# Kernel tuning notes

Hardware: AMD Instinct MI355X
Metric: run time of the kernel (lower is better)

## Reference

```python
import jax, jax.numpy as jnp
from jax import lax
import numpy as np

B, T, C, W = 128, 64, 64, 27
H, K = 128, 3
EPS = 1e-5


def _conv1d(x, w, b):
    # x: (N, Cin, W), w: (Cout, Cin, K) -> (N, Cout, W), 'same' padding
    y = lax.conv_general_dilated(x, w, (1,), 'SAME', dimension_numbers=('NCH', 'OIH', 'NCH'))
    return y + b[None, :, None]


def _mish(x):
    return x * jnp.tanh(jax.nn.softplus(x))


def _gru_layer(x_seq, act_seq, gw, gb, cw, cb, aw, ab, bn_g, bn_b):
    # x_seq: (T, B, Cin, W); act_seq: (T, B, 8, W)
    Hd = bn_g.shape[0]

    def step(h, xa):
        x, a = xa
        gates = _conv1d(jnp.concatenate([x, h], axis=1), gw, gb)  # (B, 2H, W)
        reset = jax.nn.sigmoid(gates[:, :Hd])
        update = jax.nn.sigmoid(gates[:, Hd:])
        cnm = _conv1d(jnp.concatenate([x, reset * h], axis=1), cw, cb) + _conv1d(a, aw, ab)
        pre = _mish((1.0 - update) * h + update * cnm)
        # BatchNorm1d (training mode): per-channel stats over (batch, width)
        mean = pre.mean(axis=(0, 2), keepdims=True)
        var = pre.var(axis=(0, 2), keepdims=True)
        h_next = bn_g[None, :, None] * (pre - mean) * lax.rsqrt(var + EPS) + bn_b[None, :, None]
        return h_next, h_next

    h0 = jnp.zeros((x_seq.shape[1], Hd, x_seq.shape[3]), dtype=x_seq.dtype)
    _, ys = lax.scan(step, h0, (x_seq, act_seq))
    return ys  # (T, B, H, W)


def setup_inputs():
    key = jax.random.key(0)
    ks = jax.random.split(key, 16)
    s = 0.05
    d = {}
    d['input_tensor'] = jax.random.normal(ks[0], (B, T, C, W), dtype=jnp.float32)
    # layer 0 (cur_input_dim = C)
    d['gates_w0'] = jax.random.normal(ks[1], (2 * H, C + H, K)) * s
    d['gates_b0'] = jnp.zeros((2 * H,))
    d['can_w0'] = jax.random.normal(ks[2], (H, C + H, K)) * s
    d['can_b0'] = jnp.zeros((H,))
    d['cond_w0'] = jax.random.normal(ks[3], (H, 8, K)) * s
    d['cond_b0'] = jnp.zeros((H,))
    d['bn_g0'] = jnp.ones((H,))
    d['bn_b0'] = jnp.zeros((H,))
    # layer 1 (cur_input_dim = H)
    d['gates_w1'] = jax.random.normal(ks[4], (2 * H, H + H, K)) * s
    d['gates_b1'] = jnp.zeros((2 * H,))
    d['can_w1'] = jax.random.normal(ks[5], (H, H + H, K)) * s
    d['can_b1'] = jnp.zeros((H,))
    d['cond_w1'] = jax.random.normal(ks[6], (H, 8, K)) * s
    d['cond_b1'] = jnp.zeros((H,))
    d['bn_g1'] = jnp.ones((H,))
    d['bn_b1'] = jnp.zeros((H,))
    # concentrate linear: (27*H) -> 1
    d['conc_w'] = jax.random.normal(ks[7], (1, W * H)) * s
    d['conc_b'] = jnp.zeros((1,))
    return d


def reference(input_tensor, gates_w0, gates_b0, can_w0, can_b0, cond_w0, cond_b0, bn_g0, bn_b0,
              gates_w1, gates_b1, can_w1, can_b1, cond_w1, cond_b1, bn_g1, bn_b1, conc_w, conc_b):
    x_t = jnp.transpose(input_tensor, (1, 0, 2, 3))  # (T, B, C, W)
    act_t = x_t[:, :, -8:, :]                        # (T, B, 8, W)
    h1 = _gru_layer(x_t, act_t, gates_w0, gates_b0, can_w0, can_b0, cond_w0, cond_b0, bn_g0, bn_b0)
    h2 = _gru_layer(h1, act_t, gates_w1, gates_b1, can_w1, can_b1, cond_w1, cond_b1, bn_g1, bn_b1)
    # (T, B, H, W) -> (B, T, H*W)
    out = jnp.transpose(h2, (1, 0, 2, 3)).reshape(input_tensor.shape[0], input_tensor.shape[1], -1)
    reward = out @ conc_w.T[:, 0] + conc_b[0]        # (B, T)
    return 0.99 * (reward[:, -1] - reward[:, -2])
```

## Files before the change

kernel.cpp:

```cpp
#include <hip/hip_runtime.h>
#include <math.h>

#define Bn 128
#define Tn 64
#define Cn 64
#define Wn 27
#define Hn 128
#define EPSf 1e-5f
#define NBWf 3456.0f

struct Params {
  const float* in;
  const float4* wt_g0; const float* gb0;
  const float4* wt_c0; const float* cb0;
  const float4* wt_a0; const float* ab0;
  const float* bg0; const float* bb0;
  const float4* wt_g1; const float* gb1;
  const float4* wt_c1; const float* cb1;
  const float4* wt_a1; const float* ab1;
  const float* bg1; const float* bb1;
  const float* concw;
  float* pre1a; float* pre1b; float* pre2a; float* pre2b;
  float* sums;
  unsigned* cnt;
  float* out;
};

__device__ __forceinline__ void bn_coef(const float* __restrict__ sums,
                                        const float* __restrict__ g,
                                        const float* __restrict__ b,
                                        int c, float& sc, float& sh) {
  float s1 = sums[2 * c], s2 = sums[2 * c + 1];
  float mean = s1 * (1.0f / NBWf);
  float var = s2 * (1.0f / NBWf) - mean * mean;
  sc = g[c] * rsqrtf(var + EPSf);
  sh = b[c] - mean * sc;
}

__device__ __forceinline__ float sigm(float x) {
  return 1.0f / (1.0f + __expf(-x));
}

__device__ __forceinline__ int swz(int row, int c) {
  return row * 32 + ((((c >> 2) ^ (row & 7)) & 7) << 2) + (c & 3);
}

__device__ __forceinline__ void conv_row(const float* __restrict__ rowbase,
                                         int sw, float w0, float w1, float w2,
                                         float* __restrict__ acc) {
  const float4* rp = (const float4*)rowbase;
  float xa[16];
  {
    float4 v0 = rp[0 ^ sw];
    float4 v1 = rp[1 ^ sw];
    float4 v2 = rp[2 ^ sw];
    float4 v3 = rp[3 ^ sw];
    xa[0] = v0.x; xa[1] = v0.y; xa[2] = v0.z; xa[3] = v0.w;
    xa[4] = v1.x; xa[5] = v1.y; xa[6] = v1.z; xa[7] = v1.w;
    xa[8] = v2.x; xa[9] = v2.y; xa[10] = v2.z; xa[11] = v2.w;
    xa[12] = v3.x; xa[13] = v3.y; xa[14] = v3.z; xa[15] = v3.w;
  }
#pragma unroll
  for (int c = 1; c <= 14; ++c)
    acc[c - 1] = fmaf(w2, xa[c + 1], fmaf(w1, xa[c], fmaf(w0, xa[c - 1], acc[c - 1])));
  float xc[15];
  xc[0] = xa[14]; xc[1] = xa[15];
  {
    float4 v4 = rp[4 ^ sw];
    float4 v5 = rp[5 ^ sw];
    float4 v6 = rp[6 ^ sw];
    float4 v7 = rp[7 ^ sw];
    xc[2] = v4.x; xc[3] = v4.y; xc[4] = v4.z; xc[5] = v4.w;
    xc[6] = v5.x; xc[7] = v5.y; xc[8] = v5.z; xc[9] = v5.w;
    xc[10] = v6.x; xc[11] = v6.y; xc[12] = v6.z; xc[13] = v6.w;
    xc[14] = v7.x;
  }
#pragma unroll
  for (int k = 0; k < 13; ++k)
    acc[14 + k] = fmaf(w2, xc[k + 2], fmaf(w1, xc[k + 1], fmaf(w0, xc[k], acc[14 + k])));
}

template <int IC, bool XN>
__device__ void step_body(const Params& p, int b, int t, bool hv,
    const float* __restrict__ xpre, const float* __restrict__ xs,
    const float* __restrict__ xg, const float* __restrict__ xb,
    const float* __restrict__ hpre, const float* __restrict__ hs,
    const float* __restrict__ hg, const float* __restrict__ hb,
    const float4* __restrict__ wtg, const float* __restrict__ gbias,
    const float4* __restrict__ wtc, const float* __restrict__ cbias,
    const float4* __restrict__ wta, const float* __restrict__ abias,
    float* __restrict__ pre_out, float* __restrict__ sums_out,
    float* lx, float* lrh, float* lu) {
  const int tid = threadIdx.x;
  constexpr int ROWS = IC + 136;
  {
    const int q = tid & 3;
    const int w0c = q * 7;
    const int wcnt = (q == 3) ? 6 : 7;
    for (int r = tid >> 2; r < ROWS; r += 256) {
      float sc = 1.f, sh = 0.f;
      const float* src = nullptr;
      if (r < IC) {
        if (XN) {
          bn_coef(xs, xg, xb, r, sc, sh);
          src = xpre + ((size_t)b * Hn + r) * Wn;
        } else {
          src = p.in + (((size_t)b * Tn + t) * Cn + r) * Wn;
        }
      } else if (r < IC + 128) {
        if (hv) {
          bn_coef(hs, hg, hb, r - IC, sc, sh);
          src = hpre + ((size_t)b * Hn + (r - IC)) * Wn;
        }
      } else {
        src = p.in + (((size_t)b * Tn + t) * Cn + 56 + (r - IC - 128)) * Wn;
      }
      if (q == 0) lx[swz(r, 0)] = 0.f;
      if (q == 3) {
        lx[swz(r, 28)] = 0.f; lx[swz(r, 29)] = 0.f;
        lx[swz(r, 30)] = 0.f; lx[swz(r, 31)] = 0.f;
      }
      if (src) {
        for (int j = 0; j < wcnt; ++j) {
          float v = __builtin_nontemporal_load(src + w0c + j);
          lx[swz(r, 1 + w0c + j)] = v * sc + sh;
        }
      } else {
        for (int j = 0; j < wcnt; ++j) lx[swz(r, 1 + w0c + j)] = 0.f;
      }
    }
  }
  __syncthreads();
  {
    const int rc = tid & 3;
    const int och = tid >> 2;
    float acc[27];
#pragma unroll
    for (int j = 0; j < 27; ++j) acc[j] = 0.f;
    const int rows = hv ? IC + 128 : IC;
    for (int i = rc; i < rows; i += 4) {
      float4 w = wtg[i * 256 + och];
      conv_row(lx + i * 32, i & 7, w.x, w.y, w.z, acc);
    }
#pragma unroll
    for (int j = 0; j < 27; ++j) {
      acc[j] += __shfl_xor(acc[j], 1);
      acc[j] += __shfl_xor(acc[j], 2);
    }
    if (rc == 0) {
      const float bias = gbias[och];
      if (och < 128) {
        lrh[swz(och, 0)] = 0.f;
        lrh[swz(och, 28)] = 0.f; lrh[swz(och, 29)] = 0.f;
        lrh[swz(och, 30)] = 0.f; lrh[swz(och, 31)] = 0.f;
#pragma unroll
        for (int c = 1; c <= 27; ++c) {
          float gv = sigm(acc[c - 1] + bias);
          lrh[swz(och, c)] = gv * lx[swz(IC + och, c)];
        }
      } else {
        const int ch = och - 128;
#pragma unroll
        for (int c = 1; c <= 27; ++c)
          lu[ch * 27 + (c - 1)] = sigm(acc[c - 1] + bias);
      }
    }
  }
  __syncthreads();
  {
    const int rc8 = tid & 7;
    const int ch = tid >> 3;
    float acc[27];
#pragma unroll
    for (int j = 0; j < 27; ++j) acc[j] = 0.f;
    for (int i = rc8; i < IC; i += 8) {
      float4 w = wtc[i * 128 + ch];
      conv_row(lx + i * 32, i & 7, w.x, w.y, w.z, acc);
    }
    if (hv) {
      for (int i = rc8; i < 128; i += 8) {
        float4 w = wtc[(IC + i) * 128 + ch];
        conv_row(lrh + i * 32, i & 7, w.x, w.y, w.z, acc);
      }
    }
    {
      const int i = rc8;
      float4 w = wta[i * 128 + ch];
      const int r = IC + 128 + i;
      conv_row(lx + r * 32, r & 7, w.x, w.y, w.z, acc);
    }
#pragma unroll
    for (int j = 0; j < 27; ++j) {
      acc[j] += __shfl_xor(acc[j], 1);
      acc[j] += __shfl_xor(acc[j], 2);
      acc[j] += __shfl_xor(acc[j], 4);
    }
    if (rc8 == 0) {
      const float cb = cbias[ch] + abias[ch];
      float s1 = 0.f, s2 = 0.f;
#pragma unroll
      for (int c = 1; c <= 27; ++c) {
        float u = lu[ch * 27 + (c - 1)];
        float hn = lx[swz(IC + ch, c)];
        float z = (1.f - u) * hn + u * (acc[c - 1] + cb);
        float pv;
        if (z > 20.f) {
          pv = z;
        } else {
          float q = 1.f + __expf(z);
          float q2 = q * q;
          pv = z * (q2 - 1.f) / (q2 + 1.f);
        }
        __builtin_nontemporal_store(pv,
            pre_out + ((size_t)b * Hn + ch) * Wn + (c - 1));
        s1 += pv;
        s2 += pv * pv;
      }
      atomicAdd(&sums_out[2 * ch], s1);
      atomicAdd(&sums_out[2 * ch + 1], s2);
    }
  }
}

__device__ __forceinline__ void gbar(unsigned* cnt, unsigned target) {
  __syncthreads();
  if (threadIdx.x == 0) {
    __threadfence();
    atomicAdd(cnt, 1u);
    while (__hip_atomic_load(cnt, __ATOMIC_RELAXED, __HIP_MEMORY_SCOPE_AGENT) < target) {
      __builtin_amdgcn_s_sleep(8);
    }
    __threadfence();
  }
  __syncthreads();
}

__global__ __launch_bounds__(1024, 2) void k_all(Params p) {
  __shared__ __align__(16) float lx[264 * 32];
  __shared__ __align__(16) float lrh[128 * 32];
  __shared__ float lu[128 * 27];
  const int bid = blockIdx.x;
  const bool L1b = bid >= 128;
  const int b = L1b ? bid - 128 : bid;
  float* pre1[2] = {p.pre1a, p.pre1b};
  float* pre2[2] = {p.pre2a, p.pre2b};
  for (int ph = 0; ph < 65; ++ph) {
    if (!L1b) {
      if (ph < 64) {
        const int t = ph;
        const bool hv = t > 0;
        step_body<Cn, false>(p, b, t, hv,
            nullptr, nullptr, nullptr, nullptr,
            hv ? pre1[(t - 1) & 1] : nullptr,
            hv ? p.sums + (size_t)(t - 1) * 256 : nullptr, p.bg0, p.bb0,
            p.wt_g0, p.gb0, p.wt_c0, p.cb0, p.wt_a0, p.ab0,
            pre1[t & 1], p.sums + (size_t)t * 256, lx, lrh, lu);
      }
    } else {
      if (ph >= 1) {
        const int t = ph - 1;
        const bool hv = t > 0;
        step_body<Hn, true>(p, b, t, hv,
            pre1[t & 1], p.sums + (size_t)t * 256, p.bg0, p.bb0,
            hv ? pre2[(t - 1) & 1] : nullptr,
            hv ? p.sums + (size_t)(64 + t - 1) * 256 : nullptr, p.bg1, p.bb1,
            p.wt_g1, p.gb1, p.wt_c1, p.cb1, p.wt_a1, p.ab1,
            pre2[t & 1], p.sums + (size_t)(64 + t) * 256, lx, lrh, lu);
      }
    }
    gbar(p.cnt, (unsigned)(ph + 1) * 256u);
  }
  if (!L1b) {
    const float* p63 = pre2[1];
    const float* p62 = pre2[0];
    const float* s63 = p.sums + (size_t)(64 + 63) * 256;
    const float* s62 = p.sums + (size_t)(64 + 62) * 256;
    const int tid = threadIdx.x;
    float acc = 0.f;
    for (int idx = tid; idx < Hn * Wn; idx += 1024) {
      int o = idx / Wn;
      float sc3, sh3, sc2, sh2;
      bn_coef(s63, p.bg1, p.bb1, o, sc3, sh3);
      bn_coef(s62, p.bg1, p.bb1, o, sc2, sh2);
      float v3 = p63[(size_t)b * Hn * Wn + idx] * sc3 + sh3;
      float v2 = p62[(size_t)b * Hn * Wn + idx] * sc2 + sh2;
      acc += (v3 - v2) * p.concw[idx];
    }
    lx[tid] = acc;
    __syncthreads();
    for (int s = 512; s > 0; s >>= 1) {
      if (tid < s) lx[tid] += lx[tid + s];
      __syncthreads();
    }
    if (tid == 0) p.out[b] = 0.99f * lx[0];
  }
}

__global__ void k_twt4(const float* __restrict__ src, float4* __restrict__ dst,
                       int M, int IC) {
  int idx = blockIdx.x * 256 + threadIdx.x;
  int total = M * IC;
  if (idx >= total) return;
  int i = idx / M;
  int o = idx - i * M;
  const float* s = src + ((size_t)o * IC + i) * 3;
  dst[idx] = make_float4(s[0], s[1], s[2], 0.f);
}

extern "C" void kernel_launch(void* const* d_in, const int* in_sizes, int n_in,
                              void* d_out, int out_size, void* d_ws,
                              size_t ws_size, hipStream_t stream) {
  const float* in = (const float*)d_in[0];
  const float* gw0 = (const float*)d_in[1];
  const float* gb0 = (const float*)d_in[2];
  const float* cw0 = (const float*)d_in[3];
  const float* cb0 = (const float*)d_in[4];
  const float* aw0 = (const float*)d_in[5];
  const float* ab0 = (const float*)d_in[6];
  const float* bg0 = (const float*)d_in[7];
  const float* bb0 = (const float*)d_in[8];
  const float* gw1 = (const float*)d_in[9];
  const float* gb1 = (const float*)d_in[10];
  const float* cw1 = (const float*)d_in[11];
  const float* cb1 = (const float*)d_in[12];
  const float* aw1 = (const float*)d_in[13];
  const float* ab1 = (const float*)d_in[14];
  const float* bg1 = (const float*)d_in[15];
  const float* bb1 = (const float*)d_in[16];
  const float* concw = (const float*)d_in[17];
  float* out = (float*)d_out;

  float* ws = (float*)d_ws;
  size_t off = 0;
  float4* wt_g0 = (float4*)(ws + off); off += 4 * 192 * 256;
  float4* wt_c0 = (float4*)(ws + off); off += 4 * 192 * 128;
  float4* wt_a0 = (float4*)(ws + off); off += 4 * 8 * 128;
  float4* wt_g1 = (float4*)(ws + off); off += 4 * 256 * 256;
  float4* wt_c1 = (float4*)(ws + off); off += 4 * 256 * 128;
  float4* wt_a1 = (float4*)(ws + off); off += 4 * 8 * 128;
  const size_t PRE = (size_t)Bn * Hn * Wn;
  float* pre1a = ws + off; off += PRE;
  float* pre1b = ws + off; off += PRE;
  float* pre2a = ws + off; off += PRE;
  float* pre2b = ws + off; off += PRE;
  float* sums = ws + off; off += 2 * 64 * 256;
  unsigned* cnt = (unsigned*)(ws + off); off += 16;
  if (ws_size < off * sizeof(float)) return;

  hipMemsetAsync(sums, 0, (2 * 64 * 256 + 16) * sizeof(float), stream);

  auto tw = [&](const float* s, float4* d, int M, int IC) {
    int tot = M * IC;
    k_twt4<<<(tot + 255) / 256, 256, 0, stream>>>(s, d, M, IC);
  };
  tw(gw0, wt_g0, 256, 192);
  tw(cw0, wt_c0, 128, 192);
  tw(aw0, wt_a0, 128, 8);
  tw(gw1, wt_g1, 256, 256);
  tw(cw1, wt_c1, 128, 256);
  tw(aw1, wt_a1, 128, 8);

  Params prm;
  prm.in = in;
  prm.wt_g0 = wt_g0; prm.gb0 = gb0;
  prm.wt_c0 = wt_c0; prm.cb0 = cb0;
  prm.wt_a0 = wt_a0; prm.ab0 = ab0;
  prm.bg0 = bg0; prm.bb0 = bb0;
  prm.wt_g1 = wt_g1; prm.gb1 = gb1;
  prm.wt_c1 = wt_c1; prm.cb1 = cb1;
  prm.wt_a1 = wt_a1; prm.ab1 = ab1;
  prm.bg1 = bg1; prm.bb1 = bb1;
  prm.concw = concw;
  prm.pre1a = pre1a; prm.pre1b = pre1b;
  prm.pre2a = pre2a; prm.pre2b = pre2b;
  prm.sums = sums; prm.cnt = cnt; prm.out = out;

  k_all<<<256, 1024, 0, stream>>>(prm);
}
```

Baseline: 8.393 ms.

## Spread gate epilogues across lanes, drop nontemporal hints, interleave layer blocks

```diff
diff --git a/kernel.cpp b/kernel.cpp
--- a/kernel.cpp
+++ b/kernel.cpp
@@ -121,10 +121,8 @@
         lx[swz(r, 30)] = 0.f; lx[swz(r, 31)] = 0.f;
       }
       if (src) {
-        for (int j = 0; j < wcnt; ++j) {
-          float v = __builtin_nontemporal_load(src + w0c + j);
-          lx[swz(r, 1 + w0c + j)] = v * sc + sh;
-        }
+        for (int j = 0; j < wcnt; ++j)
+          lx[swz(r, 1 + w0c + j)] = src[w0c + j] * sc + sh;
       } else {
         for (int j = 0; j < wcnt; ++j) lx[swz(r, 1 + w0c + j)] = 0.f;
       }
@@ -147,23 +145,23 @@
       acc[j] += __shfl_xor(acc[j], 1);
       acc[j] += __shfl_xor(acc[j], 2);
     }
-    if (rc == 0) {
-      const float bias = gbias[och];
-      if (och < 128) {
+    const float bias = gbias[och];
+    if (och < 128) {
+      if (rc == 0) {
         lrh[swz(och, 0)] = 0.f;
         lrh[swz(och, 28)] = 0.f; lrh[swz(och, 29)] = 0.f;
         lrh[swz(och, 30)] = 0.f; lrh[swz(och, 31)] = 0.f;
-#pragma unroll
-        for (int c = 1; c <= 27; ++c) {
-          float gv = sigm(acc[c - 1] + bias);
-          lrh[swz(och, c)] = gv * lx[swz(IC + och, c)];
-        }
-      } else {
-        const int ch = och - 128;
-#pragma unroll
-        for (int c = 1; c <= 27; ++c)
-          lu[ch * 27 + (c - 1)] = sigm(acc[c - 1] + bias);
-      }
+      }
+#pragma unroll
+      for (int j = rc; j < 27; j += 4) {
+        float gv = sigm(acc[j] + bias);
+        lrh[swz(och, j + 1)] = gv * lx[swz(IC + och, j + 1)];
+      }
+    } else {
+      const int ch = och - 128;
+#pragma unroll
+      for (int j = rc; j < 27; j += 4)
+        lu[ch * 27 + j] = sigm(acc[j] + bias);
     }
   }
   __syncthreads();
@@ -195,27 +193,29 @@
       acc[j] += __shfl_xor(acc[j], 2);
       acc[j] += __shfl_xor(acc[j], 4);
     }
+    const float cb = cbias[ch] + abias[ch];
+    float s1 = 0.f, s2 = 0.f;
+#pragma unroll
+    for (int j = rc8; j < 27; j += 8) {
+      float u = lu[ch * 27 + j];
+      float hn = lx[swz(IC + ch, j + 1)];
+      float z = (1.f - u) * hn + u * (acc[j] + cb);
+      float pv;
+      if (z > 20.f) {
+        pv = z;
+      } else {
+        float q = 1.f + __expf(z);
+        float q2 = q * q;
+        pv = z * (q2 - 1.f) / (q2 + 1.f);
+      }
+      pre_out[((size_t)b * Hn + ch) * Wn + j] = pv;
+      s1 += pv;
+      s2 += pv * pv;
+    }
+    s1 += __shfl_xor(s1, 1); s2 += __shfl_xor(s2, 1);
+    s1 += __shfl_xor(s1, 2); s2 += __shfl_xor(s2, 2);
+    s1 += __shfl_xor(s1, 4); s2 += __shfl_xor(s2, 4);
     if (rc8 == 0) {
-      const float cb = cbias[ch] + abias[ch];
-      float s1 = 0.f, s2 = 0.f;
-#pragma unroll
-      for (int c = 1; c <= 27; ++c) {
-        float u = lu[ch * 27 + (c - 1)];
-        float hn = lx[swz(IC + ch, c)];
-        float z = (1.f - u) * hn + u * (acc[c - 1] + cb);
-        float pv;
-        if (z > 20.f) {
-          pv = z;
-        } else {
-          float q = 1.f + __expf(z);
-          float q2 = q * q;
-          pv = z * (q2 - 1.f) / (q2 + 1.f);
-        }
-        __builtin_nontemporal_store(pv,
-            pre_out + ((size_t)b * Hn + ch) * Wn + (c - 1));
-        s1 += pv;
-        s2 += pv * pv;
-      }
       atomicAdd(&sums_out[2 * ch], s1);
       atomicAdd(&sums_out[2 * ch + 1], s2);
     }
@@ -240,8 +240,8 @@
   __shared__ __align__(16) float lrh[128 * 32];
   __shared__ float lu[128 * 27];
   const int bid = blockIdx.x;
-  const bool L1b = bid >= 128;
-  const int b = L1b ? bid - 128 : bid;
+  const bool L1b = (bid & 7) >= 4;
+  const int b = (bid >> 3) * 4 + (bid & 3);
   float* pre1[2] = {p.pre1a, p.pre1b};
   float* pre2[2] = {p.pre2a, p.pre2b};
   for (int ph = 0; ph < 65; ++ph) {
```

Result: faster. 7.184 ms (-14.4%).
